# Kernel optimization log

Measured on AMD Instinct MI355X. Metric: run time of the kernel, lower is better.

Reference implementation:

```python
import jax, jax.numpy as jnp
import numpy as np

BS = 32768
NIN = 512
E = 8          # num_experts
T = 2          # num_tasks
H = 256        # num_neurons_expert
NT = 1         # num_neurons_tower


def setup_inputs() -> dict:
    key = jax.random.key(0)
    ks = jax.random.split(key, 7)
    s_in = 1.0 / np.sqrt(NIN)
    s_h = 1.0 / np.sqrt(H)
    return {
        "xv": jax.random.normal(ks[0], (BS, NIN), dtype=jnp.float32),
        "We": jax.random.uniform(ks[1], (E, NIN, H), dtype=jnp.float32, minval=-s_in, maxval=s_in),
        "be": jax.random.uniform(ks[2], (E, H), dtype=jnp.float32, minval=-s_in, maxval=s_in),
        "Wg": jax.random.uniform(ks[3], (T, NIN, E), dtype=jnp.float32, minval=-s_in, maxval=s_in),
        "bg": jax.random.uniform(ks[4], (T, E), dtype=jnp.float32, minval=-s_in, maxval=s_in),
        "Wt": jax.random.uniform(ks[5], (T, H, NT), dtype=jnp.float32, minval=-s_h, maxval=s_h),
        "bt": jax.random.uniform(ks[6], (T, NT), dtype=jnp.float32, minval=-s_h, maxval=s_h),
        "bs": BS,
    }


def reference(xv, We, be, Wg, bg, Wt, bt, bs):
    # Experts: [bs, E, H] (dropout is identity in eval mode)
    out_experts = jax.nn.relu(jnp.einsum("bi,eih->beh", xv, We) + be[None, :, :])
    # Gates: [bs, T, E], softmax over experts
    gates = jax.nn.softmax(jnp.einsum("bi,tie->bte", xv, Wg) + bg[None, :, :], axis=-1)
    # Gated combine: [bs, T, H]
    input_towers = jnp.einsum("bte,beh->bth", gates, out_experts)
    # Towers: [bs, T, NT] -> squeeze NT=1 -> [bs, T]
    out_towers = jax.nn.relu(jnp.einsum("bth,thn->btn", input_towers, Wt) + bt[None, :, :])
    out = jax.nn.sigmoid(out_towers[:, :, 0])  # [bs, T]
    return (out[:, 0], out[:, 1])
```

## Files before the change

### kernel.cpp

```cpp
#include <hip/hip_runtime.h>

typedef __attribute__((ext_vector_type(8))) short short8;
typedef __attribute__((ext_vector_type(4))) float floatx4;

#define BS   32768
#define NIN  512
#define NE   8
#define NH   256

__device__ __forceinline__ unsigned short f2bf(float f) {
  unsigned int u = __float_as_uint(f);
  u += 0x7fffu + ((u >> 16) & 1u);
  return (unsigned short)(u >> 16);
}

__global__ void prep_weT(const float* __restrict__ We, unsigned short* __restrict__ WeT) {
  int e  = blockIdx.x >> 6;
  int kc = blockIdx.x & 63;
  int h  = threadIdx.x;
  short8 pk;
#pragma unroll
  for (int j = 0; j < 8; ++j)
    pk[j] = (short)f2bf(We[e * 131072 + (kc * 8 + j) * 256 + h]);
  *reinterpret_cast<short8*>(&WeT[e * 131072 + h * 512 + kc * 8]) = pk;
}

__global__ void prep_wgT(const float* __restrict__ Wg, unsigned short* __restrict__ WgT) {
  int row = blockIdx.x;
  int t = row >> 3, e = row & 7;
  int lane = threadIdx.x;
  short8 pk;
#pragma unroll
  for (int j = 0; j < 8; ++j)
    pk[j] = (short)f2bf(Wg[t * 4096 + (lane * 8 + j) * 8 + e]);
  *reinterpret_cast<short8*>(&WgT[row * 512 + lane * 8]) = pk;
}

#define GLOAD16(SRC, DST) \
  __builtin_amdgcn_global_load_lds( \
      (const __attribute__((address_space(1))) unsigned int*)(SRC), \
      (__attribute__((address_space(3))) unsigned int*)(DST), 16, 0, 0)

__global__ __launch_bounds__(512, 2) void mmoe_main(
    const float* __restrict__ xv,
    const unsigned short* __restrict__ WeT,
    const unsigned short* __restrict__ WgT,
    const float* __restrict__ be,
    const float* __restrict__ bg,
    const float* __restrict__ Wt,
    const float* __restrict__ bt,
    float* __restrict__ out)
{
  __shared__ __attribute__((aligned(16))) unsigned char smem[131072];
  __shared__ float gates_lds[64][17];
  __shared__ float red_lds[8][32][2];

  const int tid   = threadIdx.x;
  const int wave  = tid >> 6;
  const int lane  = tid & 63;
  const int row16 = lane & 15;
  const int kgrp  = lane >> 4;
  const int wm    = wave >> 2;
  const int wn    = wave & 3;
  const int b0    = blockIdx.x * 64;

  unsigned char* buf0 = smem;
  unsigned char* bufA = smem + 65536;

#pragma unroll
  for (int i = 0; i < 8; ++i) {
    int idx = i * 512 + tid;
    int r = idx >> 6, c = idx & 63;
    const float4* src = reinterpret_cast<const float4*>(xv + (size_t)(b0 + r) * 512 + c * 8);
    float4 v0 = src[0];
    float4 v1 = src[1];
    short8 pk;
    pk[0] = (short)f2bf(v0.x); pk[1] = (short)f2bf(v0.y);
    pk[2] = (short)f2bf(v0.z); pk[3] = (short)f2bf(v0.w);
    pk[4] = (short)f2bf(v1.x); pk[5] = (short)f2bf(v1.y);
    pk[6] = (short)f2bf(v1.z); pk[7] = (short)f2bf(v1.w);
    unsigned addr = ((unsigned)(r << 10) + (unsigned)(c << 4)) ^ (unsigned)((r & 7) << 4);
    *reinterpret_cast<short8*>(&bufA[addr]) = pk;
  }

  {
#pragma unroll
    for (int i = 0; i < 8; ++i) {
      unsigned x = (unsigned)(i * 8192 + tid * 16);
      unsigned r = x >> 8;
      unsigned y = (x & 255u) ^ ((r & 15u) << 4);
      const unsigned short* src = WeT + ((0 * 256 + r) * 512 + 0 * 128 + (y >> 1));
      GLOAD16(src, buf0 + (i * 8 + wave) * 1024);
    }
  }
  __syncthreads();

  if (wave < 4) {
    floatx4 gacc = {0.f, 0.f, 0.f, 0.f};
    const unsigned abase = ((unsigned)row16 << 10) + ((unsigned)kgrp << 4) + ((unsigned)wave << 14);
    const unsigned a_swz = (unsigned)((row16 & 7) << 4);
    const unsigned short* wg_lane = WgT + row16 * 512 + kgrp * 8;
#pragma unroll
    for (int ks = 0; ks < 16; ++ks) {
      short8 af = *reinterpret_cast<const short8*>(&bufA[(abase + (unsigned)(ks << 6)) ^ a_swz]);
      short8 bf = *reinterpret_cast<const short8*>(wg_lane + ks * 32);
      gacc = __builtin_amdgcn_mfma_f32_16x16x32_bf16(af, bf, gacc, 0, 0, 0);
    }
    float bgv = bg[row16];
#pragma unroll
    for (int j = 0; j < 4; ++j) {
      float v = gacc[j] + bgv;
      float mx = v;
      mx = fmaxf(mx, __shfl_xor(mx, 1));
      mx = fmaxf(mx, __shfl_xor(mx, 2));
      mx = fmaxf(mx, __shfl_xor(mx, 4));
      float p = __expf(v - mx);
      float s = p;
      s += __shfl_xor(s, 1);
      s += __shfl_xor(s, 2);
      s += __shfl_xor(s, 4);
      gates_lds[wave * 16 + kgrp * 4 + j][row16] = p / s;
    }
  }

  short8 a_reg[2][16];
  {
    const unsigned a_swz = (unsigned)((row16 & 7) << 4);
#pragma unroll
    for (int m2 = 0; m2 < 2; ++m2) {
      const unsigned rbase = (unsigned)((wm * 2 + m2) * 16 + row16) << 10;
#pragma unroll
      for (int c = 0; c < 16; ++c)
        a_reg[m2][c] = *reinterpret_cast<const short8*>(
            &bufA[rbase + (((unsigned)(c << 6) + ((unsigned)kgrp << 4)) ^ a_swz)]);
    }
  }

  float wtv[2][4];
#pragma unroll
  for (int t = 0; t < 2; ++t)
#pragma unroll
    for (int n = 0; n < 4; ++n)
      wtv[t][n] = Wt[t * 256 + wn * 64 + n * 16 + row16];

  __syncthreads();

  float outacc[2][4][2];
#pragma unroll
  for (int m = 0; m < 2; ++m)
#pragma unroll
    for (int j = 0; j < 4; ++j) { outacc[m][j][0] = 0.f; outacc[m][j][1] = 0.f; }

  const unsigned b_swz = (unsigned)(row16 << 4);
  const unsigned b_col = (unsigned)(wn * 64 + row16);

  for (int e = 0; e < 8; ++e) {
    floatx4 acc[2][4];
#pragma unroll
    for (int m = 0; m < 2; ++m)
#pragma unroll
      for (int n = 0; n < 4; ++n) acc[m][n] = (floatx4){0.f, 0.f, 0.f, 0.f};

#pragma unroll
    for (int kc = 0; kc < 4; ++kc) {
      unsigned char* sbuf = (kc & 1) ? buf0 : bufA;
      const int ne  = (kc < 3) ? e : e + 1;
      const int nkc = (kc + 1) & 3;
      if (kc < 3 || e < 7) {
#pragma unroll
        for (int i = 0; i < 8; ++i) {
          unsigned x = (unsigned)(i * 8192 + tid * 16);
          unsigned r = x >> 8;
          unsigned y = (x & 255u) ^ ((r & 15u) << 4);
          const unsigned short* src = WeT + ((ne * 256 + (int)r) * 512 + nkc * 128 + (int)(y >> 1));
          GLOAD16(src, sbuf + (i * 8 + wave) * 1024);
        }
      }

      const unsigned char* cb = (kc & 1) ? bufA : buf0;
#pragma unroll
      for (int ks = 0; ks < 4; ++ks) {
        short8 bfv[4];
#pragma unroll
        for (int n = 0; n < 4; ++n) {
          unsigned col = b_col + (unsigned)(n * 16);
          unsigned kb  = ((unsigned)(ks * 64 + kgrp * 16)) ^ b_swz;
          bfv[n] = *reinterpret_cast<const short8*>(&cb[col * 256 + kb]);
        }
#pragma unroll
        for (int m2 = 0; m2 < 2; ++m2)
#pragma unroll
          for (int n = 0; n < 4; ++n)
            acc[m2][n] = __builtin_amdgcn_mfma_f32_16x16x32_bf16(
                a_reg[m2][kc * 4 + ks], bfv[n], acc[m2][n], 0, 0, 0);
      }
      __syncthreads();
    }

    float bev[4];
#pragma unroll
    for (int n = 0; n < 4; ++n)
      bev[n] = be[e * 256 + wn * 64 + n * 16 + row16];

#pragma unroll
    for (int m2 = 0; m2 < 2; ++m2) {
#pragma unroll
      for (int j = 0; j < 4; ++j) {
        int row = (wm * 2 + m2) * 16 + kgrp * 4 + j;
        float p0 = 0.f, p1 = 0.f;
#pragma unroll
        for (int n = 0; n < 4; ++n) {
          float r = fmaxf(acc[m2][n][j] + bev[n], 0.f);
          p0 = fmaf(r, wtv[0][n], p0);
          p1 = fmaf(r, wtv[1][n], p1);
        }
        outacc[m2][j][0] = fmaf(gates_lds[row][e],     p0, outacc[m2][j][0]);
        outacc[m2][j][1] = fmaf(gates_lds[row][8 + e], p1, outacc[m2][j][1]);
      }
    }
  }

#pragma unroll
  for (int m = 0; m < 2; ++m)
#pragma unroll
    for (int j = 0; j < 4; ++j)
#pragma unroll
      for (int t = 0; t < 2; ++t) {
        float v = outacc[m][j][t];
        v += __shfl_xor(v, 1);
        v += __shfl_xor(v, 2);
        v += __shfl_xor(v, 4);
        v += __shfl_xor(v, 8);
        outacc[m][j][t] = v;
      }
  if (row16 == 0) {
#pragma unroll
    for (int m = 0; m < 2; ++m)
#pragma unroll
      for (int j = 0; j < 4; ++j) {
        int lr = m * 16 + kgrp * 4 + j;
        red_lds[wave][lr][0] = outacc[m][j][0];
        red_lds[wave][lr][1] = outacc[m][j][1];
      }
  }
  __syncthreads();

  if (tid < 128) {
    int row = tid >> 1, t = tid & 1;
    int wmr = row >> 5, lr = row & 31;
    float s = red_lds[wmr * 4 + 0][lr][t] + red_lds[wmr * 4 + 1][lr][t]
            + red_lds[wmr * 4 + 2][lr][t] + red_lds[wmr * 4 + 3][lr][t];
    s += bt[t];
    s = fmaxf(s, 0.f);
    out[t * BS + b0 + row] = 1.f / (1.f + __expf(-s));
  }
}

extern "C" void kernel_launch(void* const* d_in, const int* in_sizes, int n_in,
                              void* d_out, int out_size, void* d_ws, size_t ws_size,
                              hipStream_t stream) {
  const float* xv = (const float*)d_in[0];
  const float* We = (const float*)d_in[1];
  const float* be = (const float*)d_in[2];
  const float* Wg = (const float*)d_in[3];
  const float* bg = (const float*)d_in[4];
  const float* Wt = (const float*)d_in[5];
  const float* bt = (const float*)d_in[6];
  float* out = (float*)d_out;

  unsigned short* WeT = (unsigned short*)d_ws;
  unsigned short* WgT = WeT + 8 * 256 * 512;

  prep_weT<<<512, 256, 0, stream>>>(We, WeT);
  prep_wgT<<<16, 64, 0, stream>>>(Wg, WgT);
  mmoe_main<<<512, 512, 0, stream>>>(xv, WeT, WgT, be, bg, Wt, bt, out);
}
```

Measured before the change: 108.3 us.

## Overlap expert-weight prefetch with MFMA via manual waitcnt and raw barriers

Replaces the per-chunk __syncthreads with raw s_barrier calls plus an explicit s_waitcnt vmcnt(8). The wait then covers only the previous chunk's global-to-LDS loads, so the next chunk's prefetch stays in flight during the MFMA loop, and the MFMA section runs at raised wave priority. The first weight chunk is now issued before the xv fp32-to-bf16 conversion so the two overlap. Expert biases are staged once into LDS, and launch bounds drop to one block per CU, which gives the register-heavy A-fragment cache more VGPRs. The risks are subtle races from the hand-written vmcnt accounting and that the compiler may reorder memory operations around the inline asm.

```diff
diff --git a/kernel.cpp b/kernel.cpp
--- a/kernel.cpp
+++ b/kernel.cpp
@@ -41,7 +41,7 @@
       (const __attribute__((address_space(1))) unsigned int*)(SRC), \
       (__attribute__((address_space(3))) unsigned int*)(DST), 16, 0, 0)
 
-__global__ __launch_bounds__(512, 2) void mmoe_main(
+__global__ __launch_bounds__(512, 1) void mmoe_main(
     const float* __restrict__ xv,
     const unsigned short* __restrict__ WeT,
     const unsigned short* __restrict__ WgT,
@@ -54,6 +54,7 @@
   __shared__ __attribute__((aligned(16))) unsigned char smem[131072];
   __shared__ float gates_lds[64][17];
   __shared__ float red_lds[8][32][2];
+  __shared__ float be_lds[2048];
 
   const int tid   = threadIdx.x;
   const int wave  = tid >> 6;
@@ -66,6 +67,15 @@
 
   unsigned char* buf0 = smem;
   unsigned char* bufA = smem + 65536;
+
+#pragma unroll
+  for (int i = 0; i < 8; ++i) {
+    unsigned x = (unsigned)(i * 8192 + tid * 16);
+    unsigned r = x >> 8;
+    unsigned y = (x & 255u) ^ ((r & 15u) << 4);
+    const unsigned short* src = WeT + ((int)r * 512 + (int)(y >> 1));
+    GLOAD16(src, buf0 + (i * 8 + wave) * 1024);
+  }
 
 #pragma unroll
   for (int i = 0; i < 8; ++i) {
@@ -83,16 +93,12 @@
     *reinterpret_cast<short8*>(&bufA[addr]) = pk;
   }
 
-  {
-#pragma unroll
-    for (int i = 0; i < 8; ++i) {
-      unsigned x = (unsigned)(i * 8192 + tid * 16);
-      unsigned r = x >> 8;
-      unsigned y = (x & 255u) ^ ((r & 15u) << 4);
-      const unsigned short* src = WeT + ((0 * 256 + r) * 512 + 0 * 128 + (y >> 1));
-      GLOAD16(src, buf0 + (i * 8 + wave) * 1024);
-    }
-  }
+#pragma unroll
+  for (int j = 0; j < 4; ++j) {
+    int idx = j * 512 + tid;
+    be_lds[idx] = be[idx];
+  }
+
   __syncthreads();
 
   if (wave < 4) {
@@ -163,10 +169,11 @@
 
 #pragma unroll
     for (int kc = 0; kc < 4; ++kc) {
-      unsigned char* sbuf = (kc & 1) ? buf0 : bufA;
-      const int ne  = (kc < 3) ? e : e + 1;
-      const int nkc = (kc + 1) & 3;
-      if (kc < 3 || e < 7) {
+      const int p = e * 4 + kc;
+      if (p < 31) {
+        unsigned char* sbuf = (p & 1) ? buf0 : bufA;
+        const int ne  = (kc < 3) ? e : e + 1;
+        const int nkc = (kc + 1) & 3;
 #pragma unroll
         for (int i = 0; i < 8; ++i) {
           unsigned x = (unsigned)(i * 8192 + tid * 16);
@@ -175,9 +182,17 @@
           const unsigned short* src = WeT + ((ne * 256 + (int)r) * 512 + nkc * 128 + (int)(y >> 1));
           GLOAD16(src, sbuf + (i * 8 + wave) * 1024);
         }
-      }
-
-      const unsigned char* cb = (kc & 1) ? bufA : buf0;
+        __builtin_amdgcn_sched_barrier(0);
+        asm volatile("s_waitcnt vmcnt(8)" ::: "memory");
+      } else {
+        asm volatile("s_waitcnt vmcnt(0)" ::: "memory");
+      }
+      __builtin_amdgcn_sched_barrier(0);
+      __builtin_amdgcn_s_barrier();
+      __builtin_amdgcn_sched_barrier(0);
+
+      const unsigned char* cb = (p & 1) ? bufA : buf0;
+      __builtin_amdgcn_s_setprio(1);
 #pragma unroll
       for (int ks = 0; ks < 4; ++ks) {
         short8 bfv[4];
@@ -194,13 +209,16 @@
             acc[m2][n] = __builtin_amdgcn_mfma_f32_16x16x32_bf16(
                 a_reg[m2][kc * 4 + ks], bfv[n], acc[m2][n], 0, 0, 0);
       }
-      __syncthreads();
+      __builtin_amdgcn_s_setprio(0);
+      __builtin_amdgcn_sched_barrier(0);
+      __builtin_amdgcn_s_barrier();
+      __builtin_amdgcn_sched_barrier(0);
     }
 
     float bev[4];
 #pragma unroll
     for (int n = 0; n < 4; ++n)
-      bev[n] = be[e * 256 + wn * 64 + n * 16 + row16];
+      bev[n] = be_lds[e * 256 + wn * 64 + n * 16 + row16];
 
 #pragma unroll
     for (int m2 = 0; m2 < 2; ++m2) {
```

Result: slower. 112.1 us (+3.5%).
